# Performance work log

Hardware: AMD Instinct MI355X
Metric: run time of the kernel (lower is better)

The kernel has to match this reference:

```python
import jax, jax.numpy as jnp
import numpy as np

N_STATE = 1024
N_HEAD = 16
HEAD_DIM = N_STATE // N_HEAD


def setup_inputs() -> dict:
    key = jax.random.key(0)
    ks = jax.random.split(key, 8)
    B, S = 8, 1500
    x = jax.random.normal(ks[0], (B, S, N_STATE), dtype=jnp.float32)
    # additive causal mask (0 on/below diagonal, -inf above), broadcast over B,H
    neg = jnp.float32(-1e9)
    mask = jnp.where(jnp.tril(jnp.ones((S, S), dtype=bool)), 0.0, neg).astype(jnp.float32)
    s = 0.02
    Wq = jax.random.normal(ks[1], (N_STATE, N_STATE), dtype=jnp.float32) * s
    bq = jnp.zeros((N_STATE,), dtype=jnp.float32)
    Wk = jax.random.normal(ks[2], (N_STATE, N_STATE), dtype=jnp.float32) * s
    Wv = jax.random.normal(ks[3], (N_STATE, N_STATE), dtype=jnp.float32) * s
    bv = jnp.zeros((N_STATE,), dtype=jnp.float32)
    Wo = jax.random.normal(ks[4], (N_STATE, N_STATE), dtype=jnp.float32) * s
    bo = jnp.zeros((N_STATE,), dtype=jnp.float32)
    return {"x": x, "mask": mask, "Wq": Wq, "bq": bq, "Wk": Wk, "Wv": Wv, "bv": bv, "Wo": Wo, "bo": bo}


def reference(x, mask, Wq, bq, Wk, Wv, bv, Wo, bo):
    B, S, _ = x.shape
    # linear projections (torch Linear: x @ W^T + b); W stored as [out, in]
    q = x @ Wq.T + bq
    k = x @ Wk.T
    v = x @ Wv.T + bv
    # [B, H, S, D]
    q = q.reshape(B, S, N_HEAD, HEAD_DIM).transpose(0, 2, 1, 3)
    k = k.reshape(B, S, N_HEAD, HEAD_DIM).transpose(0, 2, 1, 3)
    v = v.reshape(B, S, N_HEAD, HEAD_DIM).transpose(0, 2, 1, 3)
    scale = 1.0 / np.sqrt(HEAD_DIM).astype(np.float32)
    scores = jnp.einsum('bhqd,bhkd->bhqk', q, k) * scale + mask
    attn = jax.nn.softmax(scores, axis=-1)
    out = jnp.einsum('bhqk,bhkd->bhqd', attn, v)
    out = out.transpose(0, 2, 1, 3).reshape(B, S, N_STATE)
    return out @ Wo.T + bo
```

## Files before the change

### kernel.cpp

```cpp
#include <hip/hip_runtime.h>
#include <hip/hip_bf16.h>

#define N_STATE 1024
#define N_HEAD  16
#define D_HEAD  64
#define BATCH   8
#define SEQ     1500
#define ROWS    (BATCH*SEQ)
#define SVP     1536
#define MTILES  94
#define MT256   47

#define BM 128
#define BN 128
#define BK 32
#define BK2 64

typedef __bf16 bf16x8 __attribute__((ext_vector_type(8)));
typedef __bf16 bf16x4 __attribute__((ext_vector_type(4)));
typedef float  f32x4  __attribute__((ext_vector_type(4)));

__device__ __forceinline__ f32x4 mfma16(bf16x8 a, bf16x8 b, f32x4 c) {
  return __builtin_amdgcn_mfma_f32_16x16x32_bf16(a, b, c, 0, 0, 0);
}

__device__ __forceinline__ void gl_lds16(const void* g, void* l) {
  __builtin_amdgcn_global_load_lds(
      (const __attribute__((address_space(1))) unsigned int*)g,
      (__attribute__((address_space(3))) unsigned int*)l, 16, 0, 0);
}

__device__ __forceinline__ void bar() {
  __builtin_amdgcn_sched_barrier(0);
  __builtin_amdgcn_s_barrier();
  __builtin_amdgcn_sched_barrier(0);
  asm volatile("" ::: "memory");
}

__global__ __launch_bounds__(256)
void cvt_all(const float* __restrict__ x,  const float* __restrict__ wq,
             const float* __restrict__ wk, const float* __restrict__ wv,
             const float* __restrict__ wo,
             __bf16* __restrict__ xb, __bf16* __restrict__ wb)
{
  const int which = blockIdx.y;
  const float* src;
  __bf16* dst;
  size_t n;
  if (which == 0) { src = x; dst = xb; n = (size_t)ROWS * N_STATE; }
  else {
    src = (which == 1) ? wq : (which == 2) ? wk : (which == 3) ? wv : wo;
    dst = wb + (size_t)(which - 1) * N_STATE * N_STATE;
    n = (size_t)N_STATE * N_STATE;
  }
  const size_t stride = (size_t)gridDim.x * 256 * 4;
  for (size_t i = ((size_t)blockIdx.x * 256 + threadIdx.x) * 4; i < n; i += stride) {
    const f32x4 v = *(const f32x4*)(src + i);
    bf16x4 c; c[0]=(__bf16)v[0]; c[1]=(__bf16)v[1]; c[2]=(__bf16)v[2]; c[3]=(__bf16)v[3];
    *(bf16x4*)(dst + i) = c;
  }
}

__global__ __launch_bounds__(512, 2)
void qkv_big(const __bf16* __restrict__ xb, const __bf16* __restrict__ wb,
             const float* __restrict__ bq, const float* __restrict__ bv,
             __bf16* __restrict__ q_ws, __bf16* __restrict__ k_ws,
             __bf16* __restrict__ vt_ws)
{
  const int xcd = blockIdx.x & 7;
  const int jj  = blockIdx.x >> 3;
  const int nt  = jj & 3;
  const int mt  = (jj >> 2) * 8 + xcd;
  if (mt >= MT256) return;

  __shared__ __bf16 lA[2][256 * 64];
  __shared__ __bf16 lB[2][256 * 64];
  const int which = blockIdx.z;
  const __bf16* W = wb + (size_t)which * N_STATE * N_STATE;

  const int tid = threadIdx.x;
  const int lane = tid & 63, wave = tid >> 6;
  const int l15 = lane & 15, quad = lane >> 4;
  const int wr = wave & 1, wc = wave >> 1;

  f32x4 acc[8][4] = {};

  auto stage_half = [&](int kt, int st) {
    const int k0 = kt * 64;
    const int buf = kt & 1;
#pragma unroll
    for (int t = 0; t < 2; ++t) {
      const int c = (st & 1) * 16 + wave * 2 + t;
      const int s = c * 64 + lane;
      const int row = s >> 3;
      const int sw  = (lane & 7) ^ (row & 7);
      if (st < 2) {
        const int ga = min(mt * 256 + row, ROWS - 1);
        gl_lds16(xb + (size_t)ga * N_STATE + k0 + sw * 8,
                 (__bf16*)lA[buf] + c * 512);
      } else {
        const int gb = nt * 256 + row;
        gl_lds16(W + (size_t)gb * N_STATE + k0 + sw * 8,
                 (__bf16*)lB[buf] + c * 512);
      }
    }
  };

  stage_half(0, 0); stage_half(0, 1); stage_half(0, 2); stage_half(0, 3);

  for (int kt = 0; kt < N_STATE / 64; ++kt) {
    const __bf16* cA = lA[kt & 1];
    const __bf16* cB = lB[kt & 1];
    const bool pf = (kt < N_STATE / 64 - 1);

    bf16x8 af[4][2], b0[2][2], b1[2][2];

    auto read_a = [&](bf16x8 (&a)[4][2], int qm) {
#pragma unroll
      for (int i = 0; i < 4; ++i) {
        const int ra = wr * 128 + qm * 64 + i * 16 + l15;
#pragma unroll
        for (int kh = 0; kh < 2; ++kh)
          a[i][kh] = *(const bf16x8*)&cA[ra * 64 + (((kh * 4 + quad) ^ (ra & 7)) * 8)];
      }
    };
    auto read_b = [&](bf16x8 (&b)[2][2], int qn) {
#pragma unroll
      for (int j = 0; j < 2; ++j) {
        const int rb = wc * 64 + qn * 32 + j * 16 + l15;
#pragma unroll
        for (int kh = 0; kh < 2; ++kh)
          b[j][kh] = *(const bf16x8*)&cB[rb * 64 + (((kh * 4 + quad) ^ (rb & 7)) * 8)];
      }
    };
    auto do_quad = [&](bf16x8 (&a)[4][2], bf16x8 (&b)[2][2], int qm, int qn) {
      __builtin_amdgcn_s_setprio(1);
#pragma unroll
      for (int kh = 0; kh < 2; ++kh)
#pragma unroll
        for (int i = 0; i < 4; ++i)
#pragma unroll
          for (int j = 0; j < 2; ++j) {
            if (which != 2)
              acc[qm * 4 + i][qn * 2 + j] =
                  mfma16(a[i][kh], b[j][kh], acc[qm * 4 + i][qn * 2 + j]);
            else
              acc[qm * 4 + i][qn * 2 + j] =
                  mfma16(b[j][kh], a[i][kh], acc[qm * 4 + i][qn * 2 + j]);
          }
      __builtin_amdgcn_s_setprio(0);
    };

    if (pf) {
      stage_half(kt + 1, 0);
      asm volatile("s_waitcnt vmcnt(2)" ::: "memory");
    } else {
      asm volatile("s_waitcnt vmcnt(0)" ::: "memory");
    }
    bar();
    read_a(af, 0);
    read_b(b0, 0);
    do_quad(af, b0, 0, 0);
    if (pf) stage_half(kt + 1, 1);
    read_b(b1, 1);
    do_quad(af, b1, 0, 1);
    if (pf) stage_half(kt + 1, 2);
    read_a(af, 1);
    do_quad(af, b0, 1, 0);
    if (pf) stage_half(kt + 1, 3);
    do_quad(af, b1, 1, 1);
    bar();
  }

  if (which != 2) {
#pragma unroll
    for (int I = 0; I < 8; ++I) {
      const int mrow = mt * 256 + wr * 128 + I * 16 + quad * 4;
#pragma unroll
      for (int J = 0; J < 4; ++J) {
        const int col = nt * 256 + wc * 64 + J * 16 + l15;
        const int h = col >> 6, d = col & 63;
        const float badd = (which == 0) ? bq[col] : 0.0f;
        __bf16* dst = (which == 0) ? q_ws : k_ws;
#pragma unroll
        for (int r = 0; r < 4; ++r) {
          const int row = mrow + r;
          if (row < ROWS) {
            const int b = row / SEQ, s = row % SEQ;
            dst[(((size_t)(b * N_HEAD + h)) * SEQ + s) * D_HEAD + d] =
                (__bf16)(acc[I][J][r] + badd);
          }
        }
      }
    }
  } else {
#pragma unroll
    for (int I = 0; I < 8; ++I) {
      const int sg = mt * 256 + wr * 128 + I * 16 + l15;
      const bool valid = sg < ROWS;
      const int b = sg / SEQ, srow = sg % SEQ;
#pragma unroll
      for (int J = 0; J < 4; ++J) {
        const int dbase = nt * 256 + wc * 64 + J * 16 + quad * 4;
#pragma unroll
        for (int r = 0; r < 4; ++r) {
          const int d = dbase + r;
          const int h = d >> 6, dd = d & 63;
          if (valid)
            vt_ws[(((size_t)(b * N_HEAD + h)) * D_HEAD + dd) * SVP + srow] =
                (__bf16)(acc[I][J][r] + bv[d]);
        }
      }
    }
  }
}

__global__ __launch_bounds__(512, 4)
void out_db(const __bf16* __restrict__ a_in, const __bf16* __restrict__ wob,
            const float* __restrict__ bo, float* __restrict__ out)
{
  const int xcd = blockIdx.x & 7;
  const int jj  = blockIdx.x >> 3;
  const int nt  = jj & 7;
  const int mt  = (jj >> 3) * 8 + xcd;
  if (mt >= MTILES) return;

  __shared__ __bf16 lA[2][BM * BK2];
  __shared__ __bf16 lB[2][BN * BK2];
  const int tid = threadIdx.x;
  const int lane = tid & 63, wave = tid >> 6;
  const int l15 = lane & 15, quad = lane >> 4;
  const int wr = wave & 1, wc = wave >> 1;

  f32x4 acc[4][2] = {};

  auto stage = [&](int kt) {
    const int k0 = kt * BK2;
    __bf16* dA = (__bf16*)lA[kt & 1];
    __bf16* dB = (__bf16*)lB[kt & 1];
#pragma unroll
    for (int t = 0; t < 2; ++t) {
      const int c = wave * 2 + t;
      const int s = c * 64 + lane;
      const int row = s >> 3;
      const int sw  = (lane & 7) ^ (row & 7);
      const int ga = min(mt * BM + row, ROWS - 1);
      gl_lds16(a_in + (size_t)ga * N_STATE + k0 + sw * 8, dA + c * 512);
      const int gb = nt * BN + row;
      gl_lds16(wob + (size_t)gb * N_STATE + k0 + sw * 8, dB + c * 512);
    }
  };

  stage(0);
  for (int kt = 0; kt < N_STATE / BK2; ++kt) {
    if (kt < N_STATE / BK2 - 1) {
      stage(kt + 1);
      asm volatile("s_waitcnt vmcnt(4)" ::: "memory");
    } else {
      asm volatile("s_waitcnt vmcnt(0)" ::: "memory");
    }
    bar();
    const __bf16* cA = lA[kt & 1];
    const __bf16* cB = lB[kt & 1];
#pragma unroll
    for (int h = 0; h < 2; ++h) {
      bf16x8 af[4], bfr[2];
#pragma unroll
      for (int i = 0; i < 4; ++i) {
        const int ra = wr * 64 + i * 16 + l15;
        af[i] = *(const bf16x8*)&cA[ra * BK2 + (((h * 4 + quad) ^ (ra & 7)) * 8)];
      }
#pragma unroll
      for (int j = 0; j < 2; ++j) {
        const int rb = wc * 32 + j * 16 + l15;
        bfr[j] = *(const bf16x8*)&cB[rb * BK2 + (((h * 4 + quad) ^ (rb & 7)) * 8)];
      }
#pragma unroll
      for (int i = 0; i < 4; ++i)
#pragma unroll
        for (int j = 0; j < 2; ++j)
          acc[i][j] = mfma16(af[i], bfr[j], acc[i][j]);
    }
    bar();
  }

#pragma unroll
  for (int i = 0; i < 4; ++i) {
    const int mrow = mt * BM + wr * 64 + i * 16 + quad * 4;
#pragma unroll
    for (int j = 0; j < 2; ++j) {
      const int col = nt * BN + wc * 32 + j * 16 + l15;
      const float badd = bo[col];
#pragma unroll
      for (int r = 0; r < 4; ++r) {
        const int row = mrow + r;
        if (row < ROWS)
          out[(size_t)row * N_STATE + col] = acc[i][j][r] + badd;
      }
    }
  }
}

__global__ __launch_bounds__(256)
void qkv_gemm(const float* __restrict__ x,
              const float* __restrict__ Wq, const float* __restrict__ bq,
              const float* __restrict__ Wk,
              const float* __restrict__ Wv, const float* __restrict__ bv,
              __bf16* __restrict__ q_ws, __bf16* __restrict__ k_ws,
              __bf16* __restrict__ vt_ws)
{
  __shared__ __bf16 lA[BM * BK];
  __shared__ __bf16 lB[BN * BK];
  const int which = blockIdx.z;
  const float* W    = (which == 0) ? Wq : (which == 1) ? Wk : Wv;
  const float* bias = (which == 0) ? bq : (which == 2) ? bv : nullptr;

  const int mt = blockIdx.x, nt = blockIdx.y;
  const int tid = threadIdx.x;
  const int lane = tid & 63, wave = tid >> 6;
  const int l15 = lane & 15, quad = lane >> 4;
  const int wr = wave >> 1, wc = wave & 1;

  f32x4 acc[4][4] = {};

  for (int k0 = 0; k0 < N_STATE; k0 += BK) {
#pragma unroll
    for (int it = 0; it < 4; ++it) {
      const int s = tid + it * 256;
      const int row = s >> 3, seg = s & 7;
      const int ga = min(mt * BM + row, ROWS - 1);
      const f32x4 va = *(const f32x4*)(x + (size_t)ga * N_STATE + k0 + seg * 4);
      bf16x4 ca; ca[0]=(__bf16)va[0]; ca[1]=(__bf16)va[1];
                 ca[2]=(__bf16)va[2]; ca[3]=(__bf16)va[3];
      *(bf16x4*)&lA[row * BK + seg * 4] = ca;
      const int gb = nt * BM + row;
      const f32x4 vb = *(const f32x4*)(W + (size_t)gb * N_STATE + k0 + seg * 4);
      bf16x4 cb; cb[0]=(__bf16)vb[0]; cb[1]=(__bf16)vb[1];
                 cb[2]=(__bf16)vb[2]; cb[3]=(__bf16)vb[3];
      *(bf16x4*)&lB[row * BK + seg * 4] = cb;
    }
    __syncthreads();
    bf16x8 af[4], bfr[4];
#pragma unroll
    for (int i = 0; i < 4; ++i) {
      af[i]  = *(const bf16x8*)&lA[(wr * 64 + i * 16 + l15) * BK + quad * 8];
      bfr[i] = *(const bf16x8*)&lB[(wc * 64 + i * 16 + l15) * BK + quad * 8];
    }
    if (which != 2) {
#pragma unroll
      for (int i = 0; i < 4; ++i)
#pragma unroll
        for (int j = 0; j < 4; ++j)
          acc[i][j] = mfma16(af[i], bfr[j], acc[i][j]);
    } else {
#pragma unroll
      for (int i = 0; i < 4; ++i)
#pragma unroll
        for (int j = 0; j < 4; ++j)
          acc[i][j] = mfma16(bfr[j], af[i], acc[i][j]);
    }
    __syncthreads();
  }

  if (which != 2) {
#pragma unroll
    for (int i = 0; i < 4; ++i) {
      const int mrow = mt * BM + wr * 64 + i * 16 + quad * 4;
#pragma unroll
      for (int j = 0; j < 4; ++j) {
        const int col = nt * BN + wc * 64 + j * 16 + l15;
        const int h = col >> 6, d = col & 63;
        const float badd = bias ? bias[col] : 0.0f;
        __bf16* dst = (which == 0) ? q_ws : k_ws;
#pragma unroll
        for (int r = 0; r < 4; ++r) {
          const int row = mrow + r;
          if (row < ROWS) {
            const int b = row / SEQ, s = row % SEQ;
            dst[(((size_t)(b * N_HEAD + h)) * SEQ + s) * D_HEAD + d] =
                (__bf16)(acc[i][j][r] + badd);
          }
        }
      }
    }
  } else {
#pragma unroll
    for (int i = 0; i < 4; ++i) {
      const int sg = mt * BM + wr * 64 + i * 16 + l15;
      const bool valid = sg < ROWS;
      const int b = sg / SEQ, srow = sg % SEQ;
#pragma unroll
      for (int j = 0; j < 4; ++j) {
        const int dbase = nt * BN + wc * 64 + j * 16 + quad * 4;
#pragma unroll
        for (int r = 0; r < 4; ++r) {
          const int d = dbase + r;
          const int h = d >> 6, dd = d & 63;
          if (valid)
            vt_ws[(((size_t)(b * N_HEAD + h)) * D_HEAD + dd) * SVP + srow] =
                (__bf16)(acc[i][j][r] + bias[d]);
        }
      }
    }
  }
}

__global__ __launch_bounds__(256)
void flash_attn(const __bf16* __restrict__ q_ws, const __bf16* __restrict__ k_ws,
                const __bf16* __restrict__ vt_ws, __bf16* __restrict__ attn)
{
  __shared__ __align__(16) __bf16 lK[8 * 512];
  __shared__ __align__(16) __bf16 lV[8 * 512];
  __shared__ __align__(16) __bf16 lP[4 * 16 * 72];
  const int bh = blockIdx.x;
  const int qt = gridDim.y - 1 - blockIdx.y;
  const int tid = threadIdx.x, lane = tid & 63, wave = tid >> 6;
  const int l15 = lane & 15, quad = lane >> 4;
  const __bf16* Q  = q_ws  + (size_t)bh * SEQ * D_HEAD;
  const __bf16* K  = k_ws  + (size_t)bh * SEQ * D_HEAD;
  const __bf16* Vt = vt_ws + (size_t)bh * D_HEAD * SVP;
  __bf16* lPw = lP + wave * 16 * 72;

  const int q0 = qt * 64, wq0 = q0 + wave * 16;
  const int qload = min(wq0 + l15, SEQ - 1);
  const bf16x8 qa0 = *(const bf16x8*)(Q + (size_t)qload * D_HEAD + quad * 8);
  const bf16x8 qa1 = *(const bf16x8*)(Q + (size_t)qload * D_HEAD + 32 + quad * 8);

  const float NEG = -1.0e30f;
  const float scale = 0.125f;
  const int query = wq0 + l15;
  f32x4 o[4] = {};
  float m_i = NEG, l_i = 0.0f;

  const int kmax = min(q0 + 63, SEQ - 1);
  const int wqmax = wq0 + 15;

  for (int kt = 0; kt <= kmax; kt += 64) {
#pragma unroll
    for (int t = 0; t < 2; ++t) {
      const int c = wave * 2 + t;
      const int gk = min(kt + lane, SEQ - 1);
      gl_lds16(K + (size_t)gk * D_HEAD + c * 8, (__bf16*)lK + c * 512);
      gl_lds16(Vt + (size_t)lane * SVP + kt + c * 8, (__bf16*)lV + c * 512);
    }
    __syncthreads();

    if (kt <= wqmax) {
      f32x4 sg[4] = {};
      __builtin_amdgcn_s_setprio(1);
#pragma unroll
      for (int g = 0; g < 4; ++g) {
        const bf16x8 k0 = *(const bf16x8*)&lK[quad * 512 + (g * 16 + l15) * 8];
        const bf16x8 k1 = *(const bf16x8*)&lK[(4 + quad) * 512 + (g * 16 + l15) * 8];
        sg[g] = mfma16(k0, qa0, sg[g]);
        sg[g] = mfma16(k1, qa1, sg[g]);
      }
      __builtin_amdgcn_s_setprio(0);
      const bool fullvis = (kt + 63 <= wq0) && (kt + 63 < SEQ);
      float tmax = NEG;
#pragma unroll
      for (int g = 0; g < 4; ++g)
#pragma unroll
        for (int r = 0; r < 4; ++r) {
          float v = sg[g][r] * scale;
          if (!fullvis) {
            const int key = kt + g * 16 + quad * 4 + r;
            v = (key <= query && key < SEQ) ? v : NEG;
          }
          sg[g][r] = v;
          tmax = fmaxf(tmax, v);
        }
      tmax = fmaxf(tmax, __shfl_xor(tmax, 16));
      tmax = fmaxf(tmax, __shfl_xor(tmax, 32));
      if (!__all(tmax <= m_i + 8.0f)) {
        const float mnew = fmaxf(m_i, tmax);
        const float alpha = __expf(m_i - mnew);
        l_i *= alpha;
#pragma unroll
        for (int nn = 0; nn < 4; ++nn)
#pragma unroll
          for (int r = 0; r < 4; ++r) o[nn][r] *= alpha;
        m_i = mnew;
      }
      float rsum = 0.0f;
#pragma unroll
      for (int g = 0; g < 4; ++g) {
        bf16x4 pk;
#pragma unroll
        for (int r = 0; r < 4; ++r) {
          const float e = __expf(sg[g][r] - m_i);
          rsum += e;
          pk[r] = (__bf16)e;
        }
        *(bf16x4*)&lPw[l15 * 72 + g * 16 + quad * 4] = pk;
      }
      rsum += __shfl_xor(rsum, 16);
      rsum += __shfl_xor(rsum, 32);
      l_i += rsum;

      __builtin_amdgcn_s_setprio(1);
#pragma unroll
      for (int h = 0; h < 2; ++h) {
        const bf16x8 pb = *(const bf16x8*)&lPw[l15 * 72 + h * 32 + quad * 8];
#pragma unroll
        for (int nn = 0; nn < 4; ++nn) {
          const bf16x8 va =
              *(const bf16x8*)&lV[(h * 4 + quad) * 512 + (nn * 16 + l15) * 8];
          o[nn] = mfma16(va, pb, o[nn]);
        }
      }
      __builtin_amdgcn_s_setprio(0);
    }
    __syncthreads();
  }

  const int b = bh >> 4, hh = bh & 15;
  if (query < SEQ) {
    const float inv = 1.0f / l_i;
#pragma unroll
    for (int nn = 0; nn < 4; ++nn) {
      bf16x4 ov;
#pragma unroll
      for (int r = 0; r < 4; ++r) ov[r] = (__bf16)(o[nn][r] * inv);
      *(bf16x4*)&attn[(((size_t)(b * SEQ + query)) * N_HEAD + hh) * D_HEAD +
                      nn * 16 + quad * 4] = ov;
    }
  }
}

__global__ __launch_bounds__(256)
void out_gemm(const __bf16* __restrict__ a_in, const float* __restrict__ Wo,
              const float* __restrict__ bo, float* __restrict__ out)
{
  __shared__ __bf16 lA[BM * BK];
  __shared__ __bf16 lB[BN * BK];
  const int mt = blockIdx.x, nt = blockIdx.y;
  const int tid = threadIdx.x;
  const int lane = tid & 63, wave = tid >> 6;
  const int l15 = lane & 15, quad = lane >> 4;
  const int wr = wave >> 1, wc = wave & 1;

  f32x4 acc[4][4] = {};

  for (int k0 = 0; k0 < N_STATE; k0 += BK) {
#pragma unroll
    for (int it = 0; it < 2; ++it) {
      const int s = tid + it * 256;
      const int row = s >> 2, seg = s & 3;
      const int ga = min(mt * BM + row, ROWS - 1);
      *(bf16x8*)&lA[row * BK + seg * 8] =
          *(const bf16x8*)(a_in + (size_t)ga * N_STATE + k0 + seg * 8);
    }
#pragma unroll
    for (int it = 0; it < 4; ++it) {
      const int s = tid + it * 256;
      const int row = s >> 3, seg = s & 7;
      const int gb = nt * BM + row;
      const f32x4 vb = *(const f32x4*)(Wo + (size_t)gb * N_STATE + k0 + seg * 4);
      bf16x4 cb; cb[0]=(__bf16)vb[0]; cb[1]=(__bf16)vb[1];
                 cb[2]=(__bf16)vb[2]; cb[3]=(__bf16)vb[3];
      *(bf16x4*)&lB[row * BK + seg * 4] = cb;
    }
    __syncthreads();
    bf16x8 af[4], bfr[4];
#pragma unroll
    for (int i = 0; i < 4; ++i) {
      af[i]  = *(const bf16x8*)&lA[(wr * 64 + i * 16 + l15) * BK + quad * 8];
      bfr[i] = *(const bf16x8*)&lB[(wc * 64 + i * 16 + l15) * BK + quad * 8];
    }
#pragma unroll
    for (int i = 0; i < 4; ++i)
#pragma unroll
      for (int j = 0; j < 4; ++j)
        acc[i][j] = mfma16(af[i], bfr[j], acc[i][j]);
    __syncthreads();
  }

#pragma unroll
  for (int i = 0; i < 4; ++i) {
    const int mrow = mt * BM + wr * 64 + i * 16 + quad * 4;
#pragma unroll
    for (int j = 0; j < 4; ++j) {
      const int col = nt * BN + wc * 64 + j * 16 + l15;
      const float badd = bo[col];
#pragma unroll
      for (int r = 0; r < 4; ++r) {
        const int row = mrow + r;
        if (row < ROWS)
          out[(size_t)row * N_STATE + col] = acc[i][j][r] + badd;
      }
    }
  }
}

extern "C" void kernel_launch(void* const* d_in, const int* in_sizes, int n_in,
                              void* d_out, int out_size, void* d_ws, size_t ws_size,
                              hipStream_t stream) {
  const float* x  = (const float*)d_in[0];
  const float* Wq = (const float*)d_in[2];
  const float* bq = (const float*)d_in[3];
  const float* Wk = (const float*)d_in[4];
  const float* Wv = (const float*)d_in[5];
  const float* bv = (const float*)d_in[6];
  const float* Wo = (const float*)d_in[7];
  const float* bo = (const float*)d_in[8];
  float* out = (float*)d_out;

  const size_t chunk  = (size_t)ROWS * N_STATE;
  const size_t vchunk = (size_t)BATCH * N_HEAD * D_HEAD * SVP;
  const size_t wchunk = (size_t)4 * N_STATE * N_STATE;
  __bf16* q_ws  = (__bf16*)d_ws;
  __bf16* k_ws  = q_ws + chunk;
  __bf16* vt_ws = k_ws + chunk;
  __bf16* attn  = vt_ws + vchunk;
  __bf16* xb    = attn;
  __bf16* wb    = attn + chunk;
  const size_t need = (3 * chunk + vchunk + wchunk) * sizeof(__bf16);

  const int MT = (ROWS + BM - 1) / BM;
  if (ws_size >= need) {
    cvt_all<<<dim3(1024, 5), 256, 0, stream>>>(x, Wq, Wk, Wv, Wo, xb, wb);
    qkv_big<<<dim3(192, 1, 3), 512, 0, stream>>>(
        xb, wb, bq, bv, q_ws, k_ws, vt_ws);
    flash_attn<<<dim3(BATCH * N_HEAD, (SEQ + 63) / 64), 256, 0, stream>>>(
        q_ws, k_ws, vt_ws, attn);
    out_db<<<dim3(768, 1, 1), 512, 0, stream>>>(
        attn, wb + (size_t)3 * N_STATE * N_STATE, bo, out);
  } else {
    qkv_gemm<<<dim3(MT, N_STATE / BN, 3), 256, 0, stream>>>(
        x, Wq, bq, Wk, Wv, bv, q_ws, k_ws, vt_ws);
    flash_attn<<<dim3(BATCH * N_HEAD, (SEQ + 63) / 64), 256, 0, stream>>>(
        q_ws, k_ws, vt_ws, attn);
    out_gemm<<<dim3(MT, N_STATE / BN), 256, 0, stream>>>(attn, Wo, bo, out);
  }
}
```

Before: 410.7 us.

## Restructure QKV GEMM mainloop into 8-phase interleaved prefetch schedule

Replaces the QKV GEMM main loop, which had one barrier pair per k-tile, with an 8-phase schedule covering two k-tiles per iteration. Global-to-LDS loads of quarter tiles are interleaved between MFMA quadrants, with a barrier after each phase and a vmcnt wait that leaves more loads in flight. The aim is to overlap memory loads with MFMA work and smooth out the stalls at the per-tile barriers. The cost is more barriers and tighter buffer-reuse ordering, which can introduce races or extra sync overhead.

```diff
diff --git a/kernel.cpp b/kernel.cpp
--- a/kernel.cpp
+++ b/kernel.cpp
@@ -62,7 +62,7 @@
 }
 
 __global__ __launch_bounds__(512, 2)
-void qkv_big(const __bf16* __restrict__ xb, const __bf16* __restrict__ wb,
+void qkv_8ph(const __bf16* __restrict__ xb, const __bf16* __restrict__ wb,
              const float* __restrict__ bq, const float* __restrict__ bv,
              __bf16* __restrict__ q_ws, __bf16* __restrict__ k_ws,
              __bf16* __restrict__ vt_ws)
@@ -85,91 +85,116 @@
 
   f32x4 acc[8][4] = {};
 
-  auto stage_half = [&](int kt, int st) {
-    const int k0 = kt * 64;
-    const int buf = kt & 1;
+  auto stage_half = [&](int tile, bool isA, int q) {
+    const int k0 = tile * 64;
+    __bf16* dst = isA ? (__bf16*)lA[tile & 1] : (__bf16*)lB[tile & 1];
 #pragma unroll
     for (int t = 0; t < 2; ++t) {
-      const int c = (st & 1) * 16 + wave * 2 + t;
-      const int s = c * 64 + lane;
-      const int row = s >> 3;
+      const int idx = wave * 2 + t;
+      const int chunk = (idx >> 3) * 16 + (idx & 7) + q * 8;
+      const int row = chunk * 8 + (lane >> 3);
       const int sw  = (lane & 7) ^ (row & 7);
-      if (st < 2) {
+      if (isA) {
         const int ga = min(mt * 256 + row, ROWS - 1);
-        gl_lds16(xb + (size_t)ga * N_STATE + k0 + sw * 8,
-                 (__bf16*)lA[buf] + c * 512);
+        gl_lds16(xb + (size_t)ga * N_STATE + k0 + sw * 8, dst + chunk * 512);
       } else {
         const int gb = nt * 256 + row;
-        gl_lds16(W + (size_t)gb * N_STATE + k0 + sw * 8,
-                 (__bf16*)lB[buf] + c * 512);
+        gl_lds16(W + (size_t)gb * N_STATE + k0 + sw * 8, dst + chunk * 512);
       }
     }
   };
 
-  stage_half(0, 0); stage_half(0, 1); stage_half(0, 2); stage_half(0, 3);
-
-  for (int kt = 0; kt < N_STATE / 64; ++kt) {
-    const __bf16* cA = lA[kt & 1];
-    const __bf16* cB = lB[kt & 1];
-    const bool pf = (kt < N_STATE / 64 - 1);
-
-    bf16x8 af[4][2], b0[2][2], b1[2][2];
-
-    auto read_a = [&](bf16x8 (&a)[4][2], int qm) {
-#pragma unroll
-      for (int i = 0; i < 4; ++i) {
-        const int ra = wr * 128 + qm * 64 + i * 16 + l15;
-#pragma unroll
-        for (int kh = 0; kh < 2; ++kh)
-          a[i][kh] = *(const bf16x8*)&cA[ra * 64 + (((kh * 4 + quad) ^ (ra & 7)) * 8)];
-      }
-    };
-    auto read_b = [&](bf16x8 (&b)[2][2], int qn) {
-#pragma unroll
-      for (int j = 0; j < 2; ++j) {
-        const int rb = wc * 64 + qn * 32 + j * 16 + l15;
-#pragma unroll
-        for (int kh = 0; kh < 2; ++kh)
-          b[j][kh] = *(const bf16x8*)&cB[rb * 64 + (((kh * 4 + quad) ^ (rb & 7)) * 8)];
-      }
-    };
-    auto do_quad = [&](bf16x8 (&a)[4][2], bf16x8 (&b)[2][2], int qm, int qn) {
-      __builtin_amdgcn_s_setprio(1);
+  auto read_a = [&](bf16x8 (&a)[4][2], const __bf16* cA, int qm) {
+#pragma unroll
+    for (int i = 0; i < 4; ++i) {
+      const int ra = wr * 128 + qm * 64 + i * 16 + l15;
 #pragma unroll
       for (int kh = 0; kh < 2; ++kh)
-#pragma unroll
-        for (int i = 0; i < 4; ++i)
-#pragma unroll
-          for (int j = 0; j < 2; ++j) {
-            if (which != 2)
-              acc[qm * 4 + i][qn * 2 + j] =
-                  mfma16(a[i][kh], b[j][kh], acc[qm * 4 + i][qn * 2 + j]);
-            else
-              acc[qm * 4 + i][qn * 2 + j] =
-                  mfma16(b[j][kh], a[i][kh], acc[qm * 4 + i][qn * 2 + j]);
-          }
-      __builtin_amdgcn_s_setprio(0);
-    };
-
+        a[i][kh] = *(const bf16x8*)&cA[ra * 64 + (((kh * 4 + quad) ^ (ra & 7)) * 8)];
+    }
+  };
+  auto read_b = [&](bf16x8 (&b)[2][2], const __bf16* cB, int qn) {
+#pragma unroll
+    for (int j = 0; j < 2; ++j) {
+      const int rb = wc * 64 + qn * 32 + j * 16 + l15;
+#pragma unroll
+      for (int kh = 0; kh < 2; ++kh)
+        b[j][kh] = *(const bf16x8*)&cB[rb * 64 + (((kh * 4 + quad) ^ (rb & 7)) * 8)];
+    }
+  };
+  auto mma_quad = [&](bf16x8 (&a)[4][2], bf16x8 (&b)[2][2], int qm, int qn) {
+    __builtin_amdgcn_s_setprio(1);
+#pragma unroll
+    for (int kh = 0; kh < 2; ++kh)
+#pragma unroll
+      for (int i = 0; i < 4; ++i)
+#pragma unroll
+        for (int j = 0; j < 2; ++j) {
+          if (which != 2)
+            acc[qm * 4 + i][qn * 2 + j] =
+                mfma16(a[i][kh], b[j][kh], acc[qm * 4 + i][qn * 2 + j]);
+          else
+            acc[qm * 4 + i][qn * 2 + j] =
+                mfma16(b[j][kh], a[i][kh], acc[qm * 4 + i][qn * 2 + j]);
+        }
+    __builtin_amdgcn_s_setprio(0);
+  };
+
+  stage_half(0, true, 0);  stage_half(0, false, 0);
+  stage_half(0, false, 1); stage_half(0, true, 1);
+  stage_half(1, true, 0);  stage_half(1, false, 0);
+  asm volatile("s_waitcnt vmcnt(4)" ::: "memory");
+  bar();
+
+  const __bf16* cA0 = lA[0]; const __bf16* cB0 = lB[0];
+  const __bf16* cA1 = lA[1]; const __bf16* cB1 = lB[1];
+  bf16x8 a[4][2], b0[2][2], b1[2][2];
+
+  for (int i = 0; i < 8; ++i) {
+    const int t1 = 2 * i + 1, s0 = 2 * i + 2, s1 = 2 * i + 3;
+    const bool pf = (i < 7);
+    read_a(a, cA0, 0);
+    read_b(b0, cB0, 0);
+    stage_half(t1, true, 1);
+    bar();
+    mma_quad(a, b0, 0, 0);
+    read_b(b1, cB0, 1);
+    stage_half(t1, false, 1);
+    bar();
+    mma_quad(a, b1, 0, 1);
+    read_a(a, cA0, 1);
+    if (pf) stage_half(s0, true, 0);
+    bar();
+    mma_quad(a, b0, 1, 0);
     if (pf) {
-      stage_half(kt + 1, 0);
-      asm volatile("s_waitcnt vmcnt(2)" ::: "memory");
+      stage_half(s0, false, 0);
+      asm volatile("s_waitcnt vmcnt(4)" ::: "memory");
     } else {
       asm volatile("s_waitcnt vmcnt(0)" ::: "memory");
     }
     bar();
-    read_a(af, 0);
-    read_b(b0, 0);
-    do_quad(af, b0, 0, 0);
-    if (pf) stage_half(kt + 1, 1);
-    read_b(b1, 1);
-    do_quad(af, b1, 0, 1);
-    if (pf) stage_half(kt + 1, 2);
-    read_a(af, 1);
-    do_quad(af, b0, 1, 0);
-    if (pf) stage_half(kt + 1, 3);
-    do_quad(af, b1, 1, 1);
-    bar();
+    mma_quad(a, b1, 1, 1);
+    read_a(a, cA1, 0);
+    read_b(b0, cB1, 0);
+    if (pf) stage_half(s0, false, 1);
+    bar();
+    mma_quad(a, b0, 0, 0);
+    read_b(b1, cB1, 1);
+    if (pf) stage_half(s0, true, 1);
+    bar();
+    mma_quad(a, b1, 0, 1);
+    read_a(a, cA1, 1);
+    if (pf) stage_half(s1, true, 0);
+    bar();
+    mma_quad(a, b0, 1, 0);
+    if (pf) {
+      stage_half(s1, false, 0);
+      asm volatile("s_waitcnt vmcnt(4)" ::: "memory");
+    } else {
+      asm volatile("s_waitcnt vmcnt(0)" ::: "memory");
+    }
+    bar();
+    mma_quad(a, b1, 1, 1);
   }
 
   if (which != 2) {
@@ -620,7 +645,7 @@
   const int MT = (ROWS + BM - 1) / BM;
   if (ws_size >= need) {
     cvt_all<<<dim3(1024, 5), 256, 0, stream>>>(x, Wq, Wk, Wv, Wo, xb, wb);
-    qkv_big<<<dim3(192, 1, 3), 512, 0, stream>>>(
+    qkv_8ph<<<dim3(192, 1, 3), 512, 0, stream>>>(
         xb, wb, bq, bv, q_ws, k_ws, vt_ws);
     flash_attn<<<dim3(BATCH * N_HEAD, (SEQ + 63) / 64), 256, 0, stream>>>(
         q_ws, k_ws, vt_ws, attn);
```

Measured after the change: 403.7 us. About the same (-1.7%).
